# Kernel optimization log

Hardware: AMD Instinct MI355X
Metric: run time of the kernel (lower is better)

Reference implementation:

```python
import jax, jax.numpy as jnp
import numpy as np

B, T, DDYN, DSTAT, UDIM, NOBS = 512, 128, 512, 256, 128, 40


def setup_inputs() -> dict:
    key = jax.random.key(0)
    ks = jax.random.split(key, 14)
    bound = 1.0 / np.sqrt(DDYN)

    def unif(k, shape):
        return jax.random.uniform(k, shape, jnp.float32, -bound, bound)

    return {
        "z_dyn": jax.random.normal(ks[0], (B, DDYN), jnp.float32),
        "z_static": jax.random.normal(ks[1], (B, DSTAT), jnp.float32),
        "dt": jax.random.uniform(ks[2], (1, 1), jnp.float32),
        "U": jax.random.normal(ks[3], (T, B, UDIM), jnp.float32),
        # LSTMCell params (torch default init: U(-1/sqrt(d), 1/sqrt(d)))
        "Wih0": unif(ks[4], (4 * DDYN, UDIM + DSTAT)),
        "Whh0": unif(ks[5], (4 * DDYN, DDYN)),
        "bih0": unif(ks[6], (4 * DDYN,)),
        "bhh0": unif(ks[7], (4 * DDYN,)),
        "Wih1": unif(ks[8], (4 * DDYN, DDYN)),
        "Whh1": unif(ks[9], (4 * DDYN, DDYN)),
        "bih1": unif(ks[10], (4 * DDYN,)),
        "bhh1": unif(ks[11], (4 * DDYN,)),
        # output head, init randn * 1/sqrt(fan_in) as in the module
        "C": jax.random.normal(ks[12], (NOBS, DDYN), jnp.float32) * (1.0 / np.sqrt(DDYN)),
        "D": jax.random.normal(ks[13], (NOBS, UDIM), jnp.float32) * (1.0 / np.sqrt(UDIM)),
    }


def _lstm_cell(x, h, c, Wih, Whh, bih, bhh):
    # gates: [B, 4d], chunk order i, f, g, o (torch LSTMCell convention)
    gates = x @ Wih.T + bih + h @ Whh.T + bhh
    i, f, g, o = jnp.split(gates, 4, axis=-1)
    c_new = jax.nn.sigmoid(f) * c + jax.nn.sigmoid(i) * jnp.tanh(g)
    h_new = jax.nn.sigmoid(o) * jnp.tanh(c_new)
    return h_new, c_new


def reference(z_dyn, z_static, dt, U, Wih0, Whh0, bih0, bhh0, Wih1, Whh1, bih1, bhh1, C, D):
    Bb, d = z_dyn.shape
    c0 = jnp.zeros((Bb, d), z_dyn.dtype)

    def step(carry, ut):
        h, (cA, cB) = carry
        ut_dt = ut * dt
        x = jnp.concatenate([ut_dt, z_static], axis=-1)  # [B, u+static]
        # layer 0: hidden is previous step's final h (z_dyn for step 0)
        h1, c1 = _lstm_cell(x, h, cA, Wih0, Whh0, bih0, bhh0)
        # layer 1: torch code passes running h (== h1) as both input and hidden
        h2, c2 = _lstm_cell(h1, h1, cB, Wih1, Whh1, bih1, bhh1)
        yt = h2 @ C.T + ut_dt @ D.T  # [B, n_obs]
        return (h2, (c1, c2)), (h2, yt)

    _, (Z, Y) = jax.lax.scan(step, (z_dyn, (c0, c0)), U)
    return Z, Y  # [T,B,d], [T,B,n_obs] (stacked versions of the returned lists)
```

## Files before the change

kernel.cpp:

```cpp
#include <hip/hip_runtime.h>

#define BB   512
#define TT   128
#define DD   512
#define DS   256
#define UD   128
#define NO   40
#define G4   2048
#define KY   640
#define NY   48

#define NRG  8
#define NCS  32
#define LDS_W0  (640*64*2)
#define LDS_W1  (512*64*2)
#define LDSB    (LDS_W0 + LDS_W1)

typedef __bf16 bf16x8 __attribute__((ext_vector_type(8)));
typedef float  f32x4  __attribute__((ext_vector_type(4)));

__device__ __forceinline__ f32x4 mfma16(bf16x8 a, bf16x8 b, f32x4 c) {
  return __builtin_amdgcn_mfma_f32_16x16x32_bf16(a, b, c, 0, 0, 0);
}
__device__ __forceinline__ float sigm(float x)     { return 1.0f / (1.0f + __expf(-x)); }
__device__ __forceinline__ float tanhfast(float x) { return 2.0f / (1.0f + __expf(-2.0f * x)) - 1.0f; }

__device__ __forceinline__ bf16x8 cvt8(const float* __restrict__ p) {
  const float4 u0 = *reinterpret_cast<const float4*>(p);
  const float4 u1 = *reinterpret_cast<const float4*>(p + 4);
  bf16x8 r;
  r[0]=(__bf16)u0.x; r[1]=(__bf16)u0.y; r[2]=(__bf16)u0.z; r[3]=(__bf16)u0.w;
  r[4]=(__bf16)u1.x; r[5]=(__bf16)u1.y; r[6]=(__bf16)u1.z; r[7]=(__bf16)u1.w;
  return r;
}
__device__ __forceinline__ bf16x8 cvt8s(const float* __restrict__ p, float s) {
  const float4 u0 = *reinterpret_cast<const float4*>(p);
  const float4 u1 = *reinterpret_cast<const float4*>(p + 4);
  bf16x8 r;
  r[0]=(__bf16)(u0.x*s); r[1]=(__bf16)(u0.y*s); r[2]=(__bf16)(u0.z*s); r[3]=(__bf16)(u0.w*s);
  r[4]=(__bf16)(u1.x*s); r[5]=(__bf16)(u1.y*s); r[6]=(__bf16)(u1.z*s); r[7]=(__bf16)(u1.w*s);
  return r;
}
__device__ __forceinline__ bf16x8 pack2(float4 a, float4 b, float s) {
  bf16x8 r;
  r[0]=(__bf16)(a.x*s); r[1]=(__bf16)(a.y*s); r[2]=(__bf16)(a.z*s); r[3]=(__bf16)(a.w*s);
  r[4]=(__bf16)(b.x*s); r[5]=(__bf16)(b.y*s); r[6]=(__bf16)(b.z*s); r[7]=(__bf16)(b.w*s);
  return r;
}

#define G_LDIC(dst, base, IMM)                                              \
  asm volatile("global_load_dwordx4 %0, %1, off offset:" #IMM " sc0 sc1"    \
               : "=&v"(dst) : "v"(base));
#define G_LDF4(dst, base, IMM)                                              \
  asm volatile("global_load_dwordx4 %0, %1, off offset:" #IMM               \
               : "=&v"(dst) : "v"(base));
#define WAITV0                                                              \
  { asm volatile("s_waitcnt vmcnt(0)" ::: "memory");                        \
    __builtin_amdgcn_sched_barrier(0); }

#define LOADH(base)                                                         \
  G_LDIC(hh0, base, 0)    G_LDIC(hh1, base, 64)                             \
  G_LDIC(hh2, base, 128)  G_LDIC(hh3, base, 192)                            \
  G_LDIC(hh4, base, 256)  G_LDIC(hh5, base, 320)                            \
  G_LDIC(hh6, base, 384)  G_LDIC(hh7, base, 448)                            \
  G_LDIC(hh8, base, 512)  G_LDIC(hh9, base, 576)                            \
  G_LDIC(hhA, base, 640)  G_LDIC(hhB, base, 704)                            \
  G_LDIC(hhC, base, 768)  G_LDIC(hhD, base, 832)                            \
  G_LDIC(hhE, base, 896)  G_LDIC(hhF, base, 960)

__device__ __forceinline__ void st_ic(__bf16* p, float v) {
  __bf16 h = (__bf16)v;
  unsigned short us = __builtin_bit_cast(unsigned short, h);
  __hip_atomic_store((unsigned short*)p, us, __ATOMIC_RELAXED, __HIP_MEMORY_SCOPE_AGENT);
}

__global__ __launch_bounds__(256) void prep_kernel(
    const float* __restrict__ z_dyn,
    const float* __restrict__ Cw, const float* __restrict__ Dw,
    __bf16* __restrict__ CD, __bf16* __restrict__ hbuf, int* __restrict__ flags)
{
  int idx = blockIdx.x * 256 + threadIdx.x;
  if (idx < NRG * NCS * 16) flags[idx] = 0;
  if (idx < NY * KY) {
    int o = idx / KY, k = idx - o * KY;
    float v = 0.f;
    if (o < NO) v = (k < DD) ? Cw[o * DD + k] : Dw[o * UD + (k - DD)];
    CD[idx] = (__bf16)v;
  }
  if (idx < BB * DD) hbuf[idx] = (__bf16)z_dyn[idx];
}

__global__ __launch_bounds__(256) void pre0_kernel(
    const float* __restrict__ z_static, const float* __restrict__ Wih0,
    const float* __restrict__ bih0, const float* __restrict__ bhh0,
    float* __restrict__ pre0)
{
  int lane = threadIdx.x & 63, w = threadIdx.x >> 6;
  int rm = lane & 15;
  int row = blockIdx.x * 64 + w * 16 + rm;
  int j0 = blockIdx.y * 64;
  int klane = (lane >> 4) * 8;
  f32x4 acc[4] = {};
  for (int k0 = 0; k0 < DS; k0 += 32) {
    int k = k0 + klane;
    bf16x8 a = cvt8(&z_static[row * DS + k]);
#pragma unroll
    for (int cf = 0; cf < 4; ++cf) {
      int j = j0 + cf * 16 + rm;
      bf16x8 b = cvt8(&Wih0[j * (UD + DS) + UD + k]);
      acc[cf] = mfma16(a, b, acc[cf]);
    }
  }
  int rbase = blockIdx.x * 64 + w * 16 + (lane >> 4) * 4;
#pragma unroll
  for (int cf = 0; cf < 4; ++cf) {
    int j = j0 + cf * 16 + rm;
    float bj = bih0[j] + bhh0[j];
#pragma unroll
    for (int q = 0; q < 4; ++q)
      pre0[(size_t)(rbase + q) * G4 + j] = acc[cf][q] + bj;
  }
}

__device__ __forceinline__ void rg_barrier(int* myflag, int* fbase,
                                           int ep, int& budget)
{
  __syncthreads();
  if (threadIdx.x == 0)
    __hip_atomic_store(myflag, ep, __ATOMIC_RELAXED, __HIP_MEMORY_SCOPE_AGENT);
  if ((threadIdx.x & 63) < 32) {
    const int* f = fbase + (threadIdx.x & 31) * 16;
    while (__hip_atomic_load(f, __ATOMIC_RELAXED, __HIP_MEMORY_SCOPE_AGENT) < ep) {
      if (--budget < 0) break;
      __builtin_amdgcn_s_sleep(1);
    }
  }
}

__global__ __launch_bounds__(256, 1) void persist_kernel(
    const float* __restrict__ U, const float* __restrict__ dtp,
    const float* __restrict__ Wih0, const float* __restrict__ Whh0,
    const float* __restrict__ Wih1, const float* __restrict__ Whh1,
    const float* __restrict__ bih1, const float* __restrict__ bhh1,
    const float* __restrict__ pre0,
    __bf16* __restrict__ hbuf, __bf16* __restrict__ h1buf,
    int* __restrict__ flags, float* __restrict__ Z)
{
  extern __shared__ __align__(16) char smem[];
  __bf16* W0L = (__bf16*)smem;
  __bf16* W1L = (__bf16*)(smem + LDS_W0);

  const int tid = threadIdx.x;
  const int r = blockIdx.x & 7, c = blockIdx.x >> 3;
  const int c16 = c * 16;

  for (int idx = tid; idx < 64 * 640; idx += 256) {
    int col = idx / 640, k = idx - col * 640;
    int g = col >> 4, i = col & 15;
    size_t j = (size_t)(g * DD + c16 + i);
    float v = (k < UD) ? Wih0[j * (UD + DS) + k] : Whh0[j * DD + (k - UD)];
    W0L[((k >> 5) * 4 + ((k >> 3) & 3)) * 512 + col * 8 + (k & 7)] = (__bf16)v;
  }
  for (int idx = tid; idx < 64 * 512; idx += 256) {
    int col = idx >> 9, k = idx & 511;
    int g = col >> 4, i = col & 15;
    size_t j = (size_t)(g * DD + c16 + i);
    float v = Wih1[j * DD + k] + Whh1[j * DD + k];
    W1L[((k >> 5) * 4 + ((k >> 3) & 3)) * 512 + col * 8 + (k & 7)] = (__bf16)v;
  }

  const int lane = tid & 63, w = tid >> 6;
  const int rm = lane & 15, lh = lane >> 4;
  const int arow  = r * 64 + w * 16 + rm;
  const int dcol  = c16 + rm;
  const int rbase = r * 64 + w * 16 + lh * 4;

  const __bf16* w0p = W0L + lh * 512 + rm * 8;
  const __bf16* w1p = W1L + lh * 512 + rm * 8;
  const __bf16* hb  = hbuf  + (size_t)arow * DD + lh * 8;
  const __bf16* h1b = h1buf + (size_t)arow * DD + lh * 8;
  int* myflag = flags + ((r * NCS + c) * 16);
  int* fbase  = flags + (r * NCS * 16);

  float preR[4][4], b1R[4];
#pragma unroll
  for (int g = 0; g < 4; ++g) {
    b1R[g] = bih1[g * DD + dcol] + bhh1[g * DD + dcol];
#pragma unroll
    for (int q = 0; q < 4; ++q)
      preR[g][q] = pre0[(size_t)(rbase + q) * G4 + g * DD + dcol];
  }
  const float dtv = dtp[0];
  float c1v[4] = {0.f,0.f,0.f,0.f};
  float c2v[4] = {0.f,0.f,0.f,0.f};
  float fz[4] = {0.f,0.f,0.f,0.f};
  int budget = 1 << 22;

  __syncthreads();

  for (int t = 0; t < TT; ++t) {
    {
      bf16x8 hh0,hh1,hh2,hh3,hh4,hh5,hh6,hh7,hh8,hh9,hhA,hhB,hhC,hhD,hhE,hhF;
      float4 u0,u1,u2,u3,u4,u5,u6,u7;
      const float* ub = U + (size_t)t * BB * UD + (size_t)arow * UD + lh * 8;
      G_LDF4(u0, ub, 0)   G_LDF4(u1, ub, 16)
      G_LDF4(u2, ub, 128) G_LDF4(u3, ub, 144)
      G_LDF4(u4, ub, 256) G_LDF4(u5, ub, 272)
      G_LDF4(u6, ub, 384) G_LDF4(u7, ub, 400)
      LOADH(hb)
      if (t > 0) {
        float* Zp = Z + (size_t)(t - 1) * BB * DD + (size_t)rbase * DD + dcol;
#pragma unroll
        for (int q = 0; q < 4; ++q) Zp[(size_t)q * DD] = fz[q];
      }
      WAITV0
      bf16x8 au[4];
      au[0] = pack2(u0,u1,dtv); au[1] = pack2(u2,u3,dtv);
      au[2] = pack2(u4,u5,dtv); au[3] = pack2(u6,u7,dtv);
      bf16x8 hA[16] = {hh0,hh1,hh2,hh3,hh4,hh5,hh6,hh7,
                       hh8,hh9,hhA,hhB,hhC,hhD,hhE,hhF};
      f32x4 acc[4] = {};
#pragma unroll
      for (int kc = 0; kc < 4; ++kc)
#pragma unroll
        for (int g = 0; g < 4; ++g) {
          bf16x8 b = *reinterpret_cast<const bf16x8*>(w0p + kc*2048 + g*128);
          acc[g] = mfma16(au[kc], b, acc[g]);
        }
#pragma unroll
      for (int kc = 0; kc < 16; ++kc)
#pragma unroll
        for (int g = 0; g < 4; ++g) {
          bf16x8 b = *reinterpret_cast<const bf16x8*>(w0p + (kc+4)*2048 + g*128);
          acc[g] = mfma16(hA[kc], b, acc[g]);
        }
#pragma unroll
      for (int q = 0; q < 4; ++q) {
        float gi = acc[0][q] + preR[0][q];
        float gf = acc[1][q] + preR[1][q];
        float gg = acc[2][q] + preR[2][q];
        float go = acc[3][q] + preR[3][q];
        float cn = sigm(gf) * c1v[q] + sigm(gi) * tanhfast(gg);
        c1v[q] = cn;
        float hn = sigm(go) * tanhfast(cn);
        st_ic(&h1buf[(size_t)(rbase + q) * DD + dcol], hn);
      }
      WAITV0
      rg_barrier(myflag, fbase, 2 * t + 1, budget);
    }
    {
      bf16x8 hh0,hh1,hh2,hh3,hh4,hh5,hh6,hh7,hh8,hh9,hhA,hhB,hhC,hhD,hhE,hhF;
      LOADH(h1b)
      WAITV0
      bf16x8 hA[16] = {hh0,hh1,hh2,hh3,hh4,hh5,hh6,hh7,
                       hh8,hh9,hhA,hhB,hhC,hhD,hhE,hhF};
      f32x4 acc[4] = {};
#pragma unroll
      for (int kc = 0; kc < 16; ++kc)
#pragma unroll
        for (int g = 0; g < 4; ++g) {
          bf16x8 b = *reinterpret_cast<const bf16x8*>(w1p + kc*2048 + g*128);
          acc[g] = mfma16(hA[kc], b, acc[g]);
        }
#pragma unroll
      for (int q = 0; q < 4; ++q) {
        float gi = acc[0][q] + b1R[0];
        float gf = acc[1][q] + b1R[1];
        float gg = acc[2][q] + b1R[2];
        float go = acc[3][q] + b1R[3];
        float cn = sigm(gf) * c2v[q] + sigm(gi) * tanhfast(gg);
        c2v[q] = cn;
        float hn = sigm(go) * tanhfast(cn);
        fz[q] = hn;
        st_ic(&hbuf[(size_t)(rbase + q) * DD + dcol], hn);
      }
      if (t != TT - 1) {
        WAITV0
        rg_barrier(myflag, fbase, 2 * t + 2, budget);
      }
    }
  }
  {
    float* Zp = Z + (size_t)(TT - 1) * BB * DD + (size_t)rbase * DD + dcol;
#pragma unroll
    for (int q = 0; q < 4; ++q) Zp[(size_t)q * DD] = fz[q];
  }
}

__global__ __launch_bounds__(256) void y_kernel(
    const float* __restrict__ Z, const float* __restrict__ U,
    const float* __restrict__ dtp, const __bf16* __restrict__ CD,
    float* __restrict__ Y)
{
  int lane = threadIdx.x & 63, w = threadIdx.x >> 6;
  int rm = lane & 15;
  int rowbase = blockIdx.x * 128 + w * 32;
  int klane = (lane >> 4) * 8;
  float dtv = dtp[0];
  f32x4 acc[2][3] = {};
#pragma unroll
  for (int k0 = 0; k0 < KY; k0 += 32) {
    int k = k0 + klane;
    bf16x8 a[2];
#pragma unroll
    for (int rb = 0; rb < 2; ++rb) {
      int rr = rowbase + rb * 16 + rm;
      if (k0 < DD) a[rb] = cvt8(&Z[(size_t)rr * DD + k]);
      else         a[rb] = cvt8s(&U[(size_t)rr * UD + (k - DD)], dtv);
    }
#pragma unroll
    for (int cf = 0; cf < 3; ++cf) {
      bf16x8 b = *reinterpret_cast<const bf16x8*>(&CD[(size_t)(cf * 16 + rm) * KY + k]);
#pragma unroll
      for (int rb = 0; rb < 2; ++rb) acc[rb][cf] = mfma16(a[rb], b, acc[rb][cf]);
    }
  }
#pragma unroll
  for (int rb = 0; rb < 2; ++rb)
#pragma unroll
    for (int cf = 0; cf < 3; ++cf) {
      int n = cf * 16 + rm;
      if (n < NO)
#pragma unroll
        for (int q = 0; q < 4; ++q) {
          int rr = rowbase + rb * 16 + (lane >> 4) * 4 + q;
          Y[(size_t)rr * NO + n] = acc[rb][cf][q];
        }
    }
}

extern "C" void kernel_launch(void* const* d_in, const int* in_sizes, int n_in,
                              void* d_out, int out_size, void* d_ws, size_t ws_size,
                              hipStream_t stream) {
  const float* z_dyn    = (const float*)d_in[0];
  const float* z_static = (const float*)d_in[1];
  const float* dt       = (const float*)d_in[2];
  const float* U        = (const float*)d_in[3];
  const float* Wih0     = (const float*)d_in[4];
  const float* Whh0     = (const float*)d_in[5];
  const float* bih0     = (const float*)d_in[6];
  const float* bhh0     = (const float*)d_in[7];
  const float* Wih1     = (const float*)d_in[8];
  const float* Whh1     = (const float*)d_in[9];
  const float* bih1     = (const float*)d_in[10];
  const float* bhh1     = (const float*)d_in[11];
  const float* Cw       = (const float*)d_in[12];
  const float* Dw       = (const float*)d_in[13];

  float* out = (float*)d_out;
  float* Z = out;
  float* Y = out + (size_t)TT * BB * DD;

  char* p = (char*)d_ws;
  auto carve = [&](size_t bytes) {
    void* r = (void*)p;
    p += (bytes + 255) & ~(size_t)255;
    return r;
  };
  __bf16* CD     = (__bf16*)carve((size_t)NY * KY * 2);
  float*  pre0   = (float*)carve((size_t)BB * G4 * 4);
  __bf16* hbuf   = (__bf16*)carve((size_t)BB * DD * 2);
  __bf16* h1buf  = (__bf16*)carve((size_t)BB * DD * 2);
  int*    flags  = (int*)carve((size_t)NRG * NCS * 16 * 4);

  prep_kernel<<<1024, 256, 0, stream>>>(z_dyn, Cw, Dw, CD, hbuf, flags);
  pre0_kernel<<<dim3(8, 32), 256, 0, stream>>>(z_static, Wih0, bih0, bhh0, pre0);

  persist_kernel<<<256, 256, LDSB, stream>>>(
      U, dt, Wih0, Whh0, Wih1, Whh1, bih1, bhh1, pre0,
      hbuf, h1buf, flags, Z);

  y_kernel<<<512, 256, 0, stream>>>(Z, U, dt, CD, Y);
}
```

Baseline: 1.625 ms.

## Replace block-wide barrier with per-wave flag polling and prefetch U

Drops the __syncthreads-based block barrier between LSTM layers and replaces it with per-wave flags. Each wave publishes its own flag and polls the 32 flags of its row-group plane with a wave-wide vote, so waves no longer wait on each other inside a block. It also prefetches next-step U inputs right after publishing, and optionally pre-converts U to bf16 scaled by dt in a separate kernel when workspace allows. The aim is to shorten the critical path of the serial time loop, at the cost of more flag traffic, an extra conversion pass and more complex memory-ordering assumptions.

```diff
diff --git a/kernel.cpp b/kernel.cpp
--- a/kernel.cpp
+++ b/kernel.cpp
@@ -12,6 +12,7 @@
 
 #define NRG  8
 #define NCS  32
+#define NFLAGS (NRG*4*32)
 #define LDS_W0  (640*64*2)
 #define LDS_W1  (512*64*2)
 #define LDSB    (LDS_W0 + LDS_W1)
@@ -48,10 +49,10 @@
   return r;
 }
 
-#define G_LDIC(dst, base, IMM)                                              \
+#define LDIC16(dst, base, IMM)                                              \
   asm volatile("global_load_dwordx4 %0, %1, off offset:" #IMM " sc0 sc1"    \
                : "=&v"(dst) : "v"(base));
-#define G_LDF4(dst, base, IMM)                                              \
+#define LDP16(dst, base, IMM)                                               \
   asm volatile("global_load_dwordx4 %0, %1, off offset:" #IMM               \
                : "=&v"(dst) : "v"(base));
 #define WAITV0                                                              \
@@ -59,19 +60,30 @@
     __builtin_amdgcn_sched_barrier(0); }
 
 #define LOADH(base)                                                         \
-  G_LDIC(hh0, base, 0)    G_LDIC(hh1, base, 64)                             \
-  G_LDIC(hh2, base, 128)  G_LDIC(hh3, base, 192)                            \
-  G_LDIC(hh4, base, 256)  G_LDIC(hh5, base, 320)                            \
-  G_LDIC(hh6, base, 384)  G_LDIC(hh7, base, 448)                            \
-  G_LDIC(hh8, base, 512)  G_LDIC(hh9, base, 576)                            \
-  G_LDIC(hhA, base, 640)  G_LDIC(hhB, base, 704)                            \
-  G_LDIC(hhC, base, 768)  G_LDIC(hhD, base, 832)                            \
-  G_LDIC(hhE, base, 896)  G_LDIC(hhF, base, 960)
+  LDIC16(hh0, base, 0)    LDIC16(hh1, base, 64)                             \
+  LDIC16(hh2, base, 128)  LDIC16(hh3, base, 192)                            \
+  LDIC16(hh4, base, 256)  LDIC16(hh5, base, 320)                            \
+  LDIC16(hh6, base, 384)  LDIC16(hh7, base, 448)                            \
+  LDIC16(hh8, base, 512)  LDIC16(hh9, base, 576)                            \
+  LDIC16(hhA, base, 640)  LDIC16(hhB, base, 704)                            \
+  LDIC16(hhC, base, 768)  LDIC16(hhD, base, 832)                            \
+  LDIC16(hhE, base, 896)  LDIC16(hhF, base, 960)
 
 __device__ __forceinline__ void st_ic(__bf16* p, float v) {
   __bf16 h = (__bf16)v;
   unsigned short us = __builtin_bit_cast(unsigned short, h);
   __hip_atomic_store((unsigned short*)p, us, __ATOMIC_RELAXED, __HIP_MEMORY_SCOPE_AGENT);
+}
+
+__device__ __forceinline__ void wave_poll(int* fp, int ep, int lane, int& budget) {
+  for (;;) {
+    int fv = 0x7fffffff;
+    if (lane < 32)
+      fv = __hip_atomic_load(fp + lane, __ATOMIC_RELAXED, __HIP_MEMORY_SCOPE_AGENT);
+    if (__all(fv >= ep)) break;
+    if (--budget < 0) break;
+    __builtin_amdgcn_s_sleep(1);
+  }
 }
 
 __global__ __launch_bounds__(256) void prep_kernel(
@@ -80,7 +92,7 @@
     __bf16* __restrict__ CD, __bf16* __restrict__ hbuf, int* __restrict__ flags)
 {
   int idx = blockIdx.x * 256 + threadIdx.x;
-  if (idx < NRG * NCS * 16) flags[idx] = 0;
+  if (idx < NFLAGS) flags[idx] = 0;
   if (idx < NY * KY) {
     int o = idx / KY, k = idx - o * KY;
     float v = 0.f;
@@ -88,6 +100,17 @@
     CD[idx] = (__bf16)v;
   }
   if (idx < BB * DD) hbuf[idx] = (__bf16)z_dyn[idx];
+}
+
+__global__ __launch_bounds__(256) void ucvt_kernel(
+    const float* __restrict__ U, const float* __restrict__ dtp,
+    __bf16* __restrict__ Ubf)
+{
+  float dtv = dtp[0];
+  size_t i = ((size_t)blockIdx.x * 256 + threadIdx.x) * 8;
+  float4 a = *reinterpret_cast<const float4*>(U + i);
+  float4 b = *reinterpret_cast<const float4*>(U + i + 4);
+  *reinterpret_cast<bf16x8*>(Ubf + i) = pack2(a, b, dtv);
 }
 
 __global__ __launch_bounds__(256) void pre0_kernel(
@@ -122,23 +145,10 @@
   }
 }
 
-__device__ __forceinline__ void rg_barrier(int* myflag, int* fbase,
-                                           int ep, int& budget)
-{
-  __syncthreads();
-  if (threadIdx.x == 0)
-    __hip_atomic_store(myflag, ep, __ATOMIC_RELAXED, __HIP_MEMORY_SCOPE_AGENT);
-  if ((threadIdx.x & 63) < 32) {
-    const int* f = fbase + (threadIdx.x & 31) * 16;
-    while (__hip_atomic_load(f, __ATOMIC_RELAXED, __HIP_MEMORY_SCOPE_AGENT) < ep) {
-      if (--budget < 0) break;
-      __builtin_amdgcn_s_sleep(1);
-    }
-  }
-}
-
+template <bool UBF>
 __global__ __launch_bounds__(256, 1) void persist_kernel(
-    const float* __restrict__ U, const float* __restrict__ dtp,
+    const float* __restrict__ U, const __bf16* __restrict__ Ubf,
+    const float* __restrict__ dtp,
     const float* __restrict__ Wih0, const float* __restrict__ Whh0,
     const float* __restrict__ Wih1, const float* __restrict__ Whh1,
     const float* __restrict__ bih1, const float* __restrict__ bhh1,
@@ -179,8 +189,9 @@
   const __bf16* w1p = W1L + lh * 512 + rm * 8;
   const __bf16* hb  = hbuf  + (size_t)arow * DD + lh * 8;
   const __bf16* h1b = h1buf + (size_t)arow * DD + lh * 8;
-  int* myflag = flags + ((r * NCS + c) * 16);
-  int* fbase  = flags + (r * NCS * 16);
+
+  int* fplane = flags + (r * 4 + w) * 32;
+  int* myflag = fplane + c;
 
   float preR[4][4], b1R[4];
 #pragma unroll
@@ -193,30 +204,43 @@
   const float dtv = dtp[0];
   float c1v[4] = {0.f,0.f,0.f,0.f};
   float c2v[4] = {0.f,0.f,0.f,0.f};
-  float fz[4] = {0.f,0.f,0.f,0.f};
+  float fz[4]  = {0.f,0.f,0.f,0.f};
   int budget = 1 << 22;
+
+  bf16x8 au0, au1, au2, au3;
+  float4 u0,u1,u2,u3,u4,u5,u6,u7;
+  if constexpr (UBF) {
+    const __bf16* ub = Ubf + (size_t)arow * UD + lh * 8;
+    LDP16(au0, ub, 0)   LDP16(au1, ub, 64)
+    LDP16(au2, ub, 128) LDP16(au3, ub, 192)
+  } else {
+    const float* ub = U + (size_t)arow * UD + lh * 8;
+    LDP16(u0, ub, 0)   LDP16(u1, ub, 16)
+    LDP16(u2, ub, 128) LDP16(u3, ub, 144)
+    LDP16(u4, ub, 256) LDP16(u5, ub, 272)
+    LDP16(u6, ub, 384) LDP16(u7, ub, 400)
+  }
 
   __syncthreads();
 
   for (int t = 0; t < TT; ++t) {
     {
       bf16x8 hh0,hh1,hh2,hh3,hh4,hh5,hh6,hh7,hh8,hh9,hhA,hhB,hhC,hhD,hhE,hhF;
-      float4 u0,u1,u2,u3,u4,u5,u6,u7;
-      const float* ub = U + (size_t)t * BB * UD + (size_t)arow * UD + lh * 8;
-      G_LDF4(u0, ub, 0)   G_LDF4(u1, ub, 16)
-      G_LDF4(u2, ub, 128) G_LDF4(u3, ub, 144)
-      G_LDF4(u4, ub, 256) G_LDF4(u5, ub, 272)
-      G_LDF4(u6, ub, 384) G_LDF4(u7, ub, 400)
-      LOADH(hb)
       if (t > 0) {
         float* Zp = Z + (size_t)(t - 1) * BB * DD + (size_t)rbase * DD + dcol;
 #pragma unroll
         for (int q = 0; q < 4; ++q) Zp[(size_t)q * DD] = fz[q];
       }
+      if (t > 0) wave_poll(fplane, 2 * t, lane, budget);
+      LOADH(hb)
       WAITV0
       bf16x8 au[4];
-      au[0] = pack2(u0,u1,dtv); au[1] = pack2(u2,u3,dtv);
-      au[2] = pack2(u4,u5,dtv); au[3] = pack2(u6,u7,dtv);
+      if constexpr (UBF) {
+        au[0] = au0; au[1] = au1; au[2] = au2; au[3] = au3;
+      } else {
+        au[0] = pack2(u0,u1,dtv); au[1] = pack2(u2,u3,dtv);
+        au[2] = pack2(u4,u5,dtv); au[3] = pack2(u6,u7,dtv);
+      }
       bf16x8 hA[16] = {hh0,hh1,hh2,hh3,hh4,hh5,hh6,hh7,
                        hh8,hh9,hhA,hhB,hhC,hhD,hhE,hhF};
       f32x4 acc[4] = {};
@@ -246,10 +270,12 @@
         st_ic(&h1buf[(size_t)(rbase + q) * DD + dcol], hn);
       }
       WAITV0
-      rg_barrier(myflag, fbase, 2 * t + 1, budget);
+      if (lane == 0)
+        __hip_atomic_store(myflag, 2 * t + 1, __ATOMIC_RELAXED, __HIP_MEMORY_SCOPE_AGENT);
     }
     {
       bf16x8 hh0,hh1,hh2,hh3,hh4,hh5,hh6,hh7,hh8,hh9,hhA,hhB,hhC,hhD,hhE,hhF;
+      wave_poll(fplane, 2 * t + 1, lane, budget);
       LOADH(h1b)
       WAITV0
       bf16x8 hA[16] = {hh0,hh1,hh2,hh3,hh4,hh5,hh6,hh7,
@@ -276,7 +302,19 @@
       }
       if (t != TT - 1) {
         WAITV0
-        rg_barrier(myflag, fbase, 2 * t + 2, budget);
+        if (lane == 0)
+          __hip_atomic_store(myflag, 2 * t + 2, __ATOMIC_RELAXED, __HIP_MEMORY_SCOPE_AGENT);
+        if constexpr (UBF) {
+          const __bf16* ub = Ubf + ((size_t)(t + 1) * BB + arow) * UD + lh * 8;
+          LDP16(au0, ub, 0)   LDP16(au1, ub, 64)
+          LDP16(au2, ub, 128) LDP16(au3, ub, 192)
+        } else {
+          const float* ub = U + ((size_t)(t + 1) * BB + arow) * UD + lh * 8;
+          LDP16(u0, ub, 0)   LDP16(u1, ub, 16)
+          LDP16(u2, ub, 128) LDP16(u3, ub, 144)
+          LDP16(u4, ub, 256) LDP16(u5, ub, 272)
+          LDP16(u6, ub, 384) LDP16(u7, ub, 400)
+        }
       }
     }
   }
@@ -352,23 +390,33 @@
   float* Y = out + (size_t)TT * BB * DD;
 
   char* p = (char*)d_ws;
+  size_t used = 0;
   auto carve = [&](size_t bytes) {
-    void* r = (void*)p;
-    p += (bytes + 255) & ~(size_t)255;
-    return r;
+    void* ret = (void*)p;
+    size_t a = (bytes + 255) & ~(size_t)255;
+    p += a; used += a;
+    return ret;
   };
   __bf16* CD     = (__bf16*)carve((size_t)NY * KY * 2);
   float*  pre0   = (float*)carve((size_t)BB * G4 * 4);
   __bf16* hbuf   = (__bf16*)carve((size_t)BB * DD * 2);
   __bf16* h1buf  = (__bf16*)carve((size_t)BB * DD * 2);
-  int*    flags  = (int*)carve((size_t)NRG * NCS * 16 * 4);
+  int*    flags  = (int*)carve((size_t)NFLAGS * 4);
+  size_t ubytes  = (size_t)TT * BB * UD * 2;
+  bool useUbf = (ws_size >= used + ubytes + 256);
+  __bf16* Ubf = useUbf ? (__bf16*)carve(ubytes) : nullptr;
 
   prep_kernel<<<1024, 256, 0, stream>>>(z_dyn, Cw, Dw, CD, hbuf, flags);
   pre0_kernel<<<dim3(8, 32), 256, 0, stream>>>(z_static, Wih0, bih0, bhh0, pre0);
-
-  persist_kernel<<<256, 256, LDSB, stream>>>(
-      U, dt, Wih0, Whh0, Wih1, Whh1, bih1, bhh1, pre0,
-      hbuf, h1buf, flags, Z);
-
+  if (useUbf) {
+    ucvt_kernel<<<(TT * BB * UD / 8 + 255) / 256, 256, 0, stream>>>(U, dt, Ubf);
+    persist_kernel<true><<<256, 256, LDSB, stream>>>(
+        U, Ubf, dt, Wih0, Whh0, Wih1, Whh1, bih1, bhh1, pre0,
+        hbuf, h1buf, flags, Z);
+  } else {
+    persist_kernel<false><<<256, 256, LDSB, stream>>>(
+        U, nullptr, dt, Wih0, Whh0, Wih1, Whh1, bih1, bhh1, pre0,
+        hbuf, h1buf, flags, Z);
+  }
   y_kernel<<<512, 256, 0, stream>>>(Z, U, dt, CD, Y);
 }
```

Result: slower. 2.352 ms (+44.7%).
